# Kernel tuning notes

Hardware: AMD Instinct MI355X
Metric: run time of the kernel (lower is better)

The kernel has to match this reference:

```python
import jax, jax.numpy as jnp
import numpy as np

B, S, DIM = 2, 2048, 2048
NH, NKV = 16, 16
HD = 128            # constructor head_dim (full per-head dim, = 2 * self.head_dim)
HHD = HD // 2       # self.head_dim = per-stream dim = 64
ROPE_THETA = 10000.0
LAMBDA_INIT = 0.8 - 0.6 * float(np.exp(-0.3 * 0))  # block_id = 0 -> 0.2
EPS = 1e-5


def make_freq_cis(seq_len, dim, theta):
    # rotation matrices, shape (seq, dim//2, 2, 2): [[cos, -sin], [sin, cos]]
    inv = 1.0 / (theta ** (np.arange(0, dim, 2, dtype=np.float32) / dim))
    ang = np.arange(seq_len, dtype=np.float32)[:, None] * inv[None, :]
    cos, sin = np.cos(ang), np.sin(ang)
    fc = np.stack([np.stack([cos, -sin], -1), np.stack([sin, cos], -1)], -2)
    return jnp.asarray(fc, dtype=jnp.float32)


def setup_inputs() -> dict:
    key = jax.random.key(0)
    ks = jax.random.split(key, 9)
    std = DIM ** -0.5
    return {
        "x": jax.random.normal(ks[0], (B, S, DIM), jnp.float32),
        "freq_cis": make_freq_cis(S, HD, ROPE_THETA),
        "wq": jax.random.normal(ks[1], (NH * HD, DIM), jnp.float32) * std,
        "wk": jax.random.normal(ks[2], (NKV * HD, DIM), jnp.float32) * std,
        "wv": jax.random.normal(ks[3], (NKV * HD, DIM), jnp.float32) * std,
        "wo": jax.random.normal(ks[4], (DIM, NH * HD), jnp.float32) * std,
        "lambda_q1": jax.random.normal(ks[5], (HHD,), jnp.float32) * 0.1,
        "lambda_k1": jax.random.normal(ks[6], (HHD,), jnp.float32) * 0.1,
        "lambda_q2": jax.random.normal(ks[7], (HHD,), jnp.float32) * 0.1,
        "lambda_k2": jax.random.normal(ks[8], (HHD,), jnp.float32) * 0.1,
        "subln_w": jnp.ones((HD,), jnp.float32),
    }


def _rope(t, fc):
    # t: (b, s, h, d); fc: (s, d//2, 2, 2). Pairs (even, odd) rotated by 2x2 matrix.
    b, s, h, d = t.shape
    t2 = t.reshape(b, s, h, d // 2, 1, 2)
    out = (t2 * fc[None, :, None]).sum(-1)  # (b, s, h, d//2, 2)
    return out.reshape(b, s, h, d)


def _causal_attn(q, k, v):
    # q, k: (b, s, h, HHD); v: (b, s, h, HD). Flash-attn default scale = 1/sqrt(q head dim).
    scale = 1.0 / jnp.sqrt(jnp.asarray(q.shape[-1], q.dtype))
    scores = jnp.einsum('bqhd,bkhd->bhqk', q, k) * scale
    s = q.shape[1]
    causal = jnp.tril(jnp.ones((s, s), bool))
    scores = jnp.where(causal, scores, jnp.finfo(scores.dtype).min)
    p = jax.nn.softmax(scores, axis=-1)
    return jnp.einsum('bhqk,bkhd->bqhd', p, v)  # (b, s, h, HD)


def reference(x, freq_cis, wq, wk, wv, wo, lambda_q1, lambda_k1, lambda_q2, lambda_k2, subln_w):
    b, s, _ = x.shape
    xq = (x @ wq.T).reshape(b, s, NH, HD)
    xk = (x @ wk.T).reshape(b, s, NKV, HD)
    xv = (x @ wv.T).reshape(b, s, NKV, HD)
    xq = _rope(xq, freq_cis)
    xk = _rope(xk, freq_cis)
    if NKV != NH:  # GQA: repeat kv heads group-wise
        rep = NH // NKV
        xk = jnp.repeat(xk, rep, axis=2)
        xv = jnp.repeat(xv, rep, axis=2)
    # split each head into two differential streams of size HHD
    xq = xq.reshape(b, s, NH, 2, HHD)
    xk = xk.reshape(b, s, NH, 2, HHD)
    attn1 = _causal_attn(xq[:, :, :, 0], xk[:, :, :, 0], xv)
    attn2 = _causal_attn(xq[:, :, :, 1], xk[:, :, :, 1], xv)
    lam1 = jnp.exp(jnp.sum(lambda_q1 * lambda_k1))
    lam2 = jnp.exp(jnp.sum(lambda_q2 * lambda_k2))
    lam_full = lam1 - lam2 + LAMBDA_INIT
    attn = attn1 - lam_full * attn2              # (b, s, h, HD)
    attn = jnp.transpose(attn, (0, 2, 1, 3))     # faithful to torch .transpose(1, 2)
    ms = jnp.mean(jnp.square(attn), axis=-1, keepdims=True)
    attn = attn * jax.lax.rsqrt(ms + EPS) * subln_w  # RMSNorm(2*HHD)
    attn = attn * (1.0 - LAMBDA_INIT)
    # faithful to original: reshape (b, h, s, HD) row-major into (b, s, h*HD)
    attn = attn.reshape(b, s, NH * HD)
    return attn @ wo.T
```

## Files before the change

kernel.cpp:

```cpp
#include <hip/hip_runtime.h>

typedef unsigned short u16;
typedef unsigned int   u32;
typedef __attribute__((ext_vector_type(8))) short s16x8;
typedef __attribute__((ext_vector_type(4))) float f32x4;

constexpr int Bc = 2, Sc = 2048, DIMc = 2048, NHc = 16, HDc = 128, Tc = Bc * Sc;
constexpr float LAMBDA_INIT_C = 0.2f;

__device__ __forceinline__ u16 f2bf(float f) {
  union { float f; u32 u; } v; v.f = f;
  u32 r = v.u + 0x7fffu + ((v.u >> 16) & 1u);
  return (u16)(r >> 16);
}
__device__ __forceinline__ float bf2f(u16 b) {
  union { u32 u; float f; } v; v.u = ((u32)b) << 16;
  return v.f;
}
__device__ __forceinline__ f32x4 mfma16(s16x8 a, s16x8 b, f32x4 c) {
  return __builtin_amdgcn_mfma_f32_16x16x32_bf16(a, b, c, 0, 0, 0);
}

typedef const __attribute__((address_space(1))) u32 gq32;
typedef __attribute__((address_space(3))) u32 lq32;
__device__ __forceinline__ void cp16(const u16* g, u16* l) {
  __builtin_amdgcn_global_load_lds((gq32*)g, (lq32*)l, 16, 0, 0);
}

__global__ void cvt_all_kernel(const float* __restrict__ x,
                               const float* __restrict__ wq, const float* __restrict__ wk,
                               const float* __restrict__ wv, const float* __restrict__ wo,
                               u16* __restrict__ xb, u16* __restrict__ wb) {
  const int i = blockIdx.x * 256 + threadIdx.x;
  constexpr int NX = Tc * DIMc / 4;
  constexpr int PW = DIMc * DIMc / 4;
  float4 v; uint2* dst;
  if (i < NX) {
    v = ((const float4*)x)[i];
    dst = ((uint2*)xb) + i;
  } else {
    const int j = i - NX;
    const int which = j >> 20;
    const int jj = j & (PW - 1);
    const float* src = which == 0 ? wq : which == 1 ? wk : which == 2 ? wv : wo;
    v = ((const float4*)src)[jj];
    dst = ((uint2*)wb) + j;
  }
  union { u16 u[4]; uint2 p; } o;
  o.u[0] = f2bf(v.x); o.u[1] = f2bf(v.y); o.u[2] = f2bf(v.z); o.u[3] = f2bf(v.w);
  *dst = o.p;
}

template<int MODE>
__global__ __launch_bounds__(512, 2) void gemm8p(const u16* __restrict__ A,
                                                 const u16* __restrict__ Bw,
                                                 u16* __restrict__ Cb,
                                                 float* __restrict__ Cf,
                                                 int N) {
  constexpr int K = 2048, NT = K / 64;
  constexpr int BUF = 24576;
  __shared__ __align__(16) u16 L[2 * BUF];

  const int tid  = threadIdx.x;
  const int lane = tid & 63, w = tid >> 6;
  const int wm = w >> 2, wn = w & 3;
  const int l15 = lane & 15, quad = lane >> 4;

  const int gx   = gridDim.x;
  const int nwg  = gx * gridDim.y;
  const int flat = blockIdx.y * gx + blockIdx.x;
  const int swz  = (flat & 7) * (nwg >> 3) + (flat >> 3);
  const int nbase = (swz % gx) * 256;
  const int mbase = (swz / gx) * 128;

  const u16* Ag = A  + (size_t)mbase * K;
  const u16* Bg = Bw + (size_t)nbase * K;

  u32 soff[2], dlin[2];
#pragma unroll
  for (int l = 0; l < 2; l++) {
    const int n = l * 512 + tid;
    const int r = n >> 3;
    const u32 q = (u32)((n & 7) ^ (r & 7));
    soff[l] = (u32)r * K + q * 8;
    dlin[l] = (u32)n * 8;
  }

  auto stA = [&](int kt, int bb) {
#pragma unroll
    for (int l = 0; l < 2; l++)
      cp16(Ag + (size_t)kt * 64 + soff[l], L + bb + dlin[l]);
  };
  auto stB = [&](int kt, int h, int bb) {
#pragma unroll
    for (int l = 0; l < 2; l++)
      cp16(Bg + (size_t)h * (128 * K) + (size_t)kt * 64 + soff[l],
           L + bb + 8192 + h * 8192 + dlin[l]);
  };

  const int aB  = (wm * 64 + l15) * 64;
  const int bB  = 8192 + (wn * 64 + l15) * 64;
  const int xq0 = (quad ^ (l15 & 7)) << 3;

  f32x4 acc[4][4];
#pragma unroll
  for (int i = 0; i < 4; i++)
#pragma unroll
    for (int j = 0; j < 4; j++) acc[i][j] = (f32x4){0.f, 0.f, 0.f, 0.f};

  stB(0, 0, 0); stB(0, 1, 0); stA(0, 0); stB(1, 0, BUF); stB(1, 1, BUF);
  asm volatile("s_waitcnt vmcnt(4)" ::: "memory");
  asm volatile("s_barrier" ::: "memory");

  s16x8 aL[2][2], aH[2][2], b0[2][2], b1[2][2];

  for (int kt = 0; kt < NT; ++kt) {
    const int cb  = (kt & 1) * BUF;
    const int nb  = BUF - cb;
    const int tgA = (kt + 1 < NT) ? kt + 1 : 0;
    const int tgB = (kt + 2 < NT) ? kt + 2 : 0;

#pragma unroll
    for (int i = 0; i < 2; i++) {
      aL[i][0] = *(const s16x8*)(L + cb + aB + i * 1024 + xq0);
      aL[i][1] = *(const s16x8*)(L + cb + aB + i * 1024 + (xq0 ^ 32));
    }
#pragma unroll
    for (int j = 0; j < 2; j++) {
      b0[j][0] = *(const s16x8*)(L + cb + bB + j * 1024 + xq0);
      b0[j][1] = *(const s16x8*)(L + cb + bB + j * 1024 + (xq0 ^ 32));
    }
    stA(tgA, nb);
    asm volatile("s_barrier" ::: "memory");
    asm volatile("s_waitcnt lgkmcnt(0)" ::: "memory");
    __builtin_amdgcn_sched_barrier(0);
    __builtin_amdgcn_s_setprio(1);
#pragma unroll
    for (int i = 0; i < 2; i++)
#pragma unroll
      for (int j = 0; j < 2; j++) {
        acc[i][j] = mfma16(aL[i][0], b0[j][0], acc[i][j]);
        acc[i][j] = mfma16(aL[i][1], b0[j][1], acc[i][j]);
      }
    __builtin_amdgcn_s_setprio(0);
    asm volatile("s_barrier" ::: "memory");

#pragma unroll
    for (int j = 0; j < 2; j++) {
      b1[j][0] = *(const s16x8*)(L + cb + bB + (j + 2) * 1024 + xq0);
      b1[j][1] = *(const s16x8*)(L + cb + bB + (j + 2) * 1024 + (xq0 ^ 32));
    }
    asm volatile("s_barrier" ::: "memory");
    asm volatile("s_waitcnt lgkmcnt(0)" ::: "memory");
    __builtin_amdgcn_sched_barrier(0);
    __builtin_amdgcn_s_setprio(1);
#pragma unroll
    for (int i = 0; i < 2; i++)
#pragma unroll
      for (int j = 0; j < 2; j++) {
        acc[i][j + 2] = mfma16(aL[i][0], b1[j][0], acc[i][j + 2]);
        acc[i][j + 2] = mfma16(aL[i][1], b1[j][1], acc[i][j + 2]);
      }
    __builtin_amdgcn_s_setprio(0);
    asm volatile("s_barrier" ::: "memory");

#pragma unroll
    for (int i = 0; i < 2; i++) {
      aH[i][0] = *(const s16x8*)(L + cb + aB + (i + 2) * 1024 + xq0);
      aH[i][1] = *(const s16x8*)(L + cb + aB + (i + 2) * 1024 + (xq0 ^ 32));
    }
    stB(tgB, 0, cb);
    asm volatile("s_barrier" ::: "memory");
    asm volatile("s_waitcnt lgkmcnt(0)" ::: "memory");
    __builtin_amdgcn_sched_barrier(0);
    __builtin_amdgcn_s_setprio(1);
#pragma unroll
    for (int i = 0; i < 2; i++)
#pragma unroll
      for (int j = 0; j < 2; j++) {
        acc[i + 2][j + 2] = mfma16(aH[i][0], b1[j][0], acc[i + 2][j + 2]);
        acc[i + 2][j + 2] = mfma16(aH[i][1], b1[j][1], acc[i + 2][j + 2]);
      }
    __builtin_amdgcn_s_setprio(0);
    asm volatile("s_barrier" ::: "memory");

    stB(tgB, 1, cb);
    asm volatile("s_waitcnt vmcnt(4)" ::: "memory");
    asm volatile("s_barrier" ::: "memory");
    __builtin_amdgcn_sched_barrier(0);
    __builtin_amdgcn_s_setprio(1);
#pragma unroll
    for (int i = 0; i < 2; i++)
#pragma unroll
      for (int j = 0; j < 2; j++) {
        acc[i + 2][j] = mfma16(aH[i][0], b0[j][0], acc[i + 2][j]);
        acc[i + 2][j] = mfma16(aH[i][1], b0[j][1], acc[i + 2][j]);
      }
    __builtin_amdgcn_s_setprio(0);
    asm volatile("s_barrier" ::: "memory");
  }
  asm volatile("s_waitcnt vmcnt(0)" ::: "memory");

  if (MODE == 0) {
    const int which = nbase >> 11;
    const int ncol  = nbase & 2047;
    u16* Ob = Cb + (size_t)which * ((size_t)Tc * DIMc);
#pragma unroll
    for (int i = 0; i < 4; i++) {
      const int m0 = mbase + wm * 64 + i * 16 + quad * 4;
#pragma unroll
      for (int j = 0; j < 4; j++) {
        const int n0 = ncol + wn * 64 + j * 16 + l15;
#pragma unroll
        for (int r = 0; r < 4; r++)
          Ob[(size_t)(m0 + r) * 2048 + n0] = f2bf(acc[i][j][r]);
      }
    }
  } else {
#pragma unroll
    for (int i = 0; i < 4; i++) {
      const int m0 = mbase + wm * 64 + i * 16 + quad * 4;
#pragma unroll
      for (int j = 0; j < 4; j++) {
        const int n0 = nbase + wn * 64 + j * 16 + l15;
#pragma unroll
        for (int r = 0; r < 4; r++)
          Cf[(size_t)(m0 + r) * N + n0] = acc[i][j][r];
      }
    }
  }
}

__global__ void prep_kernel(const u16* __restrict__ qg, const u16* __restrict__ kg,
                            const u16* __restrict__ vg, const float* __restrict__ fc,
                            u16* __restrict__ qr, u16* __restrict__ kr,
                            u16* __restrict__ vt) {
  __shared__ u16 tile[32][33];
  const int bid = blockIdx.x;
  if (bid < 32768) {
    const bool isq = bid < 16384;
    const u16* xg = isq ? qg : kg;
    u16* outp = isq ? qr : kr;
    const float scale = isq ? 0.125f : 1.0f;
    const int idx = (bid & 16383) * 256 + threadIdx.x;
    const int p = idx & 63;
    const int hh = (idx >> 6) & 15;
    const int tt = idx >> 10;
    const int s = tt & (Sc - 1);
    const int bb = tt >> 11;
    const float c  = fc[(size_t)(s * 64 + p) * 4 + 0] * scale;
    const float sn = fc[(size_t)(s * 64 + p) * 4 + 2] * scale;
    const u32 xp = *(const u32*)(xg + (size_t)tt * DIMc + hh * HDc + p * 2);
    const float x0 = bf2f((u16)xp), x1 = bf2f((u16)(xp >> 16));
    const u16 y0 = f2bf(c * x0 - sn * x1);
    const u16 y1 = f2bf(sn * x0 + c * x1);
    *(u32*)(outp + ((size_t)(bb * NHc + hh) * Sc + s) * HDc + p * 2) =
        (u32)y0 | ((u32)y1 << 16);
  } else {
    const int vb = bid - 32768;
    const int bh = vb >> 8;
    const int bb = bh >> 4, hh = bh & 15;
    const int rem = vb & 255;
    const int s0 = (rem & 63) * 32, d0 = (rem >> 6) * 32;
    const int tx = threadIdx.x & 31, ty = threadIdx.x >> 5;
#pragma unroll
    for (int pp = 0; pp < 4; pp++) {
      const int s = s0 + ty + pp * 8;
      tile[ty + pp * 8][tx] = vg[(size_t)(bb * Sc + s) * DIMc + hh * HDc + d0 + tx];
    }
    __syncthreads();
#pragma unroll
    for (int pp = 0; pp < 4; pp++) {
      const int d = d0 + ty + pp * 8;
      vt[((size_t)bh * HDc + d) * Sc + s0 + tx] = tile[tx][ty + pp * 8];
    }
  }
}

__global__ __launch_bounds__(256, 2) void diff_attn_kernel(
    const u16* __restrict__ qr, const u16* __restrict__ kr, const u16* __restrict__ vt,
    const float* __restrict__ lq1, const float* __restrict__ lk1,
    const float* __restrict__ lq2, const float* __restrict__ lk2,
    const float* __restrict__ subw, u16* __restrict__ Y) {
  __shared__ u16 KB[2][8192];
  __shared__ u16 VB[2][8192];

  const int h = blockIdx.y, b = blockIdx.z, jb = blockIdx.x;
  const int bh = b * NHc + h;
  const int tid = threadIdx.x;
  const int w = tid >> 6, lane = tid & 63;
  const int l15 = lane & 15, quad = lane >> 4;

  const u16* krb = kr + (size_t)bh * Sc * HDc;
  const u16* vtb = vt + (size_t)bh * HDc * Sc;

  float lp1 = lq1[lane] * lk1[lane];
  float lp2 = lq2[lane] * lk2[lane];
#pragma unroll
  for (int m = 32; m; m >>= 1) { lp1 += __shfl_xor(lp1, m); lp2 += __shfl_xor(lp2, m); }
  const float lam = __expf(lp1) - __expf(lp2) + LAMBDA_INIT_C;

  float wsub[8];
#pragma unroll
  for (int dn = 0; dn < 8; dn++) wsub[dn] = subw[dn * 16 + l15];

  size_t offK[4], offV[4];
  int dstO[4];
#pragma unroll
  for (int oo = 0; oo < 4; oo++) {
    const int n = w * 256 + oo * 64 + lane;
    const int s = n & 31, dblk = (n >> 5) & 15, sub = n >> 9;
    const int mkey = (s & 3) + ((s >> 2) & 3) * 8 + ((s >> 4) << 2);
    offK[oo] = (size_t)(sub * 32 + mkey) * HDc + dblk * 8;
    offV[oo] = (size_t)(n & 127) * Sc + (sub * 32 + ((n >> 7) & 3) * 8);
    dstO[oo] = n * 8;
  }

  for (int ph = 0; ph < 2; ph++) {
    const int t = ph ? (31 - jb) : jb;
    const int rowbase = t * 64 + w * 16;
    const int nc = t + 1;

    const u16* qp = qr + ((size_t)bh * Sc + rowbase + l15) * HDc + quad * 8;
    s16x8 qa[2][2];
    qa[0][0] = *(const s16x8*)(qp);
    qa[0][1] = *(const s16x8*)(qp + 32);
    qa[1][0] = *(const s16x8*)(qp + 64);
    qa[1][1] = *(const s16x8*)(qp + 96);

    f32x4 o[2][8];
#pragma unroll
    for (int st = 0; st < 2; st++)
#pragma unroll
      for (int dn = 0; dn < 8; dn++) o[st][dn] = (f32x4){0.f, 0.f, 0.f, 0.f};
    float lpart[2] = { 0.f, 0.f };

    __syncthreads();
#pragma unroll
    for (int oo = 0; oo < 4; oo++) cp16(krb + offK[oo], KB[0] + dstO[oo]);
#pragma unroll
    for (int oo = 0; oo < 4; oo++) cp16(vtb + offV[oo], VB[0] + dstO[oo]);

    for (int c = 0; c < nc; c++) {
      __syncthreads();
      if (c + 1 < nc) {
        const int kb1 = (c + 1) * 64;
        u16* Kn = KB[(c + 1) & 1];
        u16* Vn = VB[(c + 1) & 1];
#pragma unroll
        for (int oo = 0; oo < 4; oo++) cp16(krb + (size_t)kb1 * HDc + offK[oo], Kn + dstO[oo]);
#pragma unroll
        for (int oo = 0; oo < 4; oo++) cp16(vtb + offV[oo] + kb1, Vn + dstO[oo]);
      }
      const u16* Kb = KB[c & 1];
      const u16* Vb = VB[c & 1];
      const int kb = c * 64;
      const bool diag = (c == nc - 1);

#pragma unroll
      for (int sub = 0; sub < 2; sub++) {
        if (diag && sub == 1 && w < 2) continue;

        f32x4 sc[2][2];
#pragma unroll
        for (int st = 0; st < 2; st++)
#pragma unroll
          for (int kt = 0; kt < 2; kt++) sc[st][kt] = (f32x4){0.f, 0.f, 0.f, 0.f};
#pragma unroll
        for (int st = 0; st < 2; st++)
#pragma unroll
          for (int kh = 0; kh < 2; kh++) {
            const int base = sub * 512 + (st * 8 + kh * 4 + quad) * 32;
#pragma unroll
            for (int kt = 0; kt < 2; kt++) {
              const s16x8 kf = *(const s16x8*)(Kb + (size_t)(base + kt * 16 + l15) * 8);
              sc[st][kt] = mfma16(kf, qa[st][kh], sc[st][kt]);
            }
          }

        s16x8 pa[2];
#pragma unroll
        for (int st = 0; st < 2; st++) {
          float p[8];
#pragma unroll
          for (int kt = 0; kt < 2; kt++)
#pragma unroll
            for (int r = 0; r < 4; r++) p[kt * 4 + r] = __expf(sc[st][kt][r]);
          if (diag) {
            const int qrow = rowbase + l15;
            const int kb0 = kb + sub * 32 + quad * 8;
#pragma unroll
            for (int j8 = 0; j8 < 8; j8++)
              if (kb0 + j8 > qrow) p[j8] = 0.f;
          }
          float sm = 0.f;
#pragma unroll
          for (int j8 = 0; j8 < 8; j8++) sm += p[j8];
          lpart[st] += sm;
          union { u16 us[8]; s16x8 vv; } pk;
#pragma unroll
          for (int j8 = 0; j8 < 8; j8++) pk.us[j8] = f2bf(p[j8]);
          pa[st] = pk.vv;
        }

#pragma unroll
        for (int dn = 0; dn < 8; dn++) {
          const s16x8 vf =
              *(const s16x8*)(Vb + (size_t)(sub * 512 + quad * 128 + dn * 16 + l15) * 8);
          o[0][dn] = mfma16(pa[0], vf, o[0][dn]);
          o[1][dn] = mfma16(pa[1], vf, o[1][dn]);
        }
      }
    }

    float lL0 = lpart[0], lL1 = lpart[1];
    lL0 += __shfl_xor(lL0, 16); lL0 += __shfl_xor(lL0, 32);
    lL1 += __shfl_xor(lL1, 16); lL1 += __shfl_xor(lL1, 32);
    const float inv1 = 1.f / lL0;
    const float inv2 = lam / lL1;
    float i1C[4], i2C[4];
#pragma unroll
    for (int r = 0; r < 4; r++) {
      i1C[r] = __shfl(inv1, quad * 4 + r, 16);
      i2C[r] = __shfl(inv2, quad * 4 + r, 16);
    }
    float yv[8][4], ss[4] = { 0.f, 0.f, 0.f, 0.f };
#pragma unroll
    for (int dn = 0; dn < 8; dn++)
#pragma unroll
      for (int r = 0; r < 4; r++) {
        const float y = o[0][dn][r] * i1C[r] - o[1][dn][r] * i2C[r];
        yv[dn][r] = y;
        ss[r] += y * y;
      }
#pragma unroll
    for (int r = 0; r < 4; r++) {
#pragma unroll
      for (int mm = 1; mm < 16; mm <<= 1) ss[r] += __shfl_xor(ss[r], mm);
    }
    float scl[4];
#pragma unroll
    for (int r = 0; r < 4; r++) scl[r] = rsqrtf(ss[r] * (1.f / 128.f) + 1e-5f) * 0.8f;

    u16* yrow = Y + ((size_t)(b * Sc + h * 128 + t * 4 + w)) * 2048;
#pragma unroll
    for (int dn = 0; dn < 8; dn++)
#pragma unroll
      for (int r = 0; r < 4; r++)
        yrow[(quad * 4 + r) * 128 + dn * 16 + l15] = f2bf(yv[dn][r] * scl[r] * wsub[dn]);
  }
}

extern "C" void kernel_launch(void* const* d_in, const int* in_sizes, int n_in,
                              void* d_out, int out_size, void* d_ws, size_t ws_size,
                              hipStream_t stream) {
  const float* x    = (const float*)d_in[0];
  const float* fc   = (const float*)d_in[1];
  const float* wq   = (const float*)d_in[2];
  const float* wk   = (const float*)d_in[3];
  const float* wv   = (const float*)d_in[4];
  const float* wo   = (const float*)d_in[5];
  const float* lq1  = (const float*)d_in[6];
  const float* lk1  = (const float*)d_in[7];
  const float* lq2  = (const float*)d_in[8];
  const float* lk2  = (const float*)d_in[9];
  const float* subw = (const float*)d_in[10];
  float* out = (float*)d_out;

  char* ws = (char*)d_ws;
  constexpr size_t SZ_X  = (size_t)Tc * DIMc * 2;
  constexpr size_t SZ_W  = (size_t)DIMc * DIMc * 2;
  constexpr size_t SZ_T  = (size_t)Tc * DIMc * 2;
  u16* xb  = (u16*)(ws);
  u16* wqb = (u16*)(ws + SZ_X);
  u16* wob = (u16*)(ws + SZ_X + 3 * SZ_W);
  u16* qg  = (u16*)(ws + SZ_X + 4 * SZ_W);
  u16* kg  = (u16*)(ws + SZ_X + 4 * SZ_W + SZ_T);
  u16* vg  = (u16*)(ws + SZ_X + 4 * SZ_W + 2 * SZ_T);
  u16* qr  = (u16*)(ws + SZ_X + 4 * SZ_W + 3 * SZ_T);
  u16* kr  = (u16*)(ws + SZ_X + 4 * SZ_W + 4 * SZ_T);
  u16* vt  = (u16*)(ws + SZ_X + 4 * SZ_W + 5 * SZ_T);
  u16* Y   = (u16*)(ws + SZ_X + 4 * SZ_W + 6 * SZ_T);

  cvt_all_kernel<<<(Tc * DIMc / 4 + 4 * DIMc * DIMc / 4) / 256, 256, 0, stream>>>(
      x, wq, wk, wv, wo, xb, wqb);

  gemm8p<0><<<dim3(DIMc * 3 / 256, Tc / 128), 512, 0, stream>>>(
      xb, wqb, qg, nullptr, 3 * DIMc);

  prep_kernel<<<16384 + 16384 + 8192, 256, 0, stream>>>(qg, kg, vg, fc, qr, kr, vt);

  diff_attn_kernel<<<dim3(16, NHc, Bc), 256, 0, stream>>>(
      qr, kr, vt, lq1, lk1, lq2, lk2, subw, Y);

  gemm8p<1><<<dim3(DIMc / 256, Tc / 128), 512, 0, stream>>>(
      Y, wob, nullptr, out, DIMc);
}
```

Measured before the change: 412.7 us.

## Enlarge GEMM block tile to 256x256 with 8x4 per-wave accumulators

The bf16 GEMM grows its workgroup tile from 128x256 to 256x256. Each wave now accumulates a 128x64 sub-tile, so every B fragment read from LDS feeds twice as many MFMAs and global traffic per FLOP falls. The A and B prefetch is restructured to load whole k-tiles two steps ahead into double buffers (64 KB each), and the block-index swizzle now runs M-major. The costs are twice the LDS per block, more accumulator registers (which may drop occupancy below the declared two blocks per CU), and half as many workgroups, which can leave CUs idle on the smaller output-projection GEMM.

```diff
diff --git a/kernel.cpp b/kernel.cpp
--- a/kernel.cpp
+++ b/kernel.cpp
@@ -55,10 +55,9 @@
 __global__ __launch_bounds__(512, 2) void gemm8p(const u16* __restrict__ A,
                                                  const u16* __restrict__ Bw,
                                                  u16* __restrict__ Cb,
-                                                 float* __restrict__ Cf,
-                                                 int N) {
+                                                 float* __restrict__ Cf) {
   constexpr int K = 2048, NT = K / 64;
-  constexpr int BUF = 24576;
+  constexpr int BUF = 32768;
   __shared__ __align__(16) u16 L[2 * BUF];
 
   const int tid  = threadIdx.x;
@@ -66,19 +65,19 @@
   const int wm = w >> 2, wn = w & 3;
   const int l15 = lane & 15, quad = lane >> 4;
 
-  const int gx   = gridDim.x;
-  const int nwg  = gx * gridDim.y;
-  const int flat = blockIdx.y * gx + blockIdx.x;
+  const int mt   = gridDim.y;
+  const int nwg  = gridDim.x * mt;
+  const int flat = blockIdx.x * mt + blockIdx.y;
   const int swz  = (flat & 7) * (nwg >> 3) + (flat >> 3);
-  const int nbase = (swz % gx) * 256;
-  const int mbase = (swz / gx) * 128;
+  const int nbase = (swz / mt) * 256;
+  const int mbase = (swz % mt) * 256;
 
   const u16* Ag = A  + (size_t)mbase * K;
   const u16* Bg = Bw + (size_t)nbase * K;
 
-  u32 soff[2], dlin[2];
-#pragma unroll
-  for (int l = 0; l < 2; l++) {
+  u32 soff[4], dlin[4];
+#pragma unroll
+  for (int l = 0; l < 4; l++) {
     const int n = l * 512 + tid;
     const int r = n >> 3;
     const u32 q = (u32)((n & 7) ^ (r & 7));
@@ -88,59 +87,55 @@
 
   auto stA = [&](int kt, int bb) {
 #pragma unroll
-    for (int l = 0; l < 2; l++)
+    for (int l = 0; l < 4; l++)
       cp16(Ag + (size_t)kt * 64 + soff[l], L + bb + dlin[l]);
   };
-  auto stB = [&](int kt, int h, int bb) {
-#pragma unroll
-    for (int l = 0; l < 2; l++)
-      cp16(Bg + (size_t)h * (128 * K) + (size_t)kt * 64 + soff[l],
-           L + bb + 8192 + h * 8192 + dlin[l]);
+  auto stB = [&](int kt, int bb) {
+#pragma unroll
+    for (int l = 0; l < 4; l++)
+      cp16(Bg + (size_t)kt * 64 + soff[l], L + bb + 16384 + dlin[l]);
   };
 
-  const int aB  = (wm * 64 + l15) * 64;
-  const int bB  = 8192 + (wn * 64 + l15) * 64;
+  const int aB  = (wm * 128 + l15) * 64;
+  const int bB  = 16384 + (wn * 64 + l15) * 64;
   const int xq0 = (quad ^ (l15 & 7)) << 3;
 
-  f32x4 acc[4][4];
-#pragma unroll
-  for (int i = 0; i < 4; i++)
+  f32x4 acc[8][4];
+#pragma unroll
+  for (int i = 0; i < 8; i++)
 #pragma unroll
     for (int j = 0; j < 4; j++) acc[i][j] = (f32x4){0.f, 0.f, 0.f, 0.f};
 
-  stB(0, 0, 0); stB(0, 1, 0); stA(0, 0); stB(1, 0, BUF); stB(1, 1, BUF);
-  asm volatile("s_waitcnt vmcnt(4)" ::: "memory");
+  stB(0, 0); stA(0, 0); stB(1, BUF); stA(1, BUF);
+  asm volatile("s_waitcnt vmcnt(8)" ::: "memory");
   asm volatile("s_barrier" ::: "memory");
 
-  s16x8 aL[2][2], aH[2][2], b0[2][2], b1[2][2];
+  s16x8 a[4][2], b0[2][2], b1[2][2];
 
   for (int kt = 0; kt < NT; ++kt) {
-    const int cb  = (kt & 1) * BUF;
-    const int nb  = BUF - cb;
-    const int tgA = (kt + 1 < NT) ? kt + 1 : 0;
-    const int tgB = (kt + 2 < NT) ? kt + 2 : 0;
-
-#pragma unroll
-    for (int i = 0; i < 2; i++) {
-      aL[i][0] = *(const s16x8*)(L + cb + aB + i * 1024 + xq0);
-      aL[i][1] = *(const s16x8*)(L + cb + aB + i * 1024 + (xq0 ^ 32));
+    const int cb = (kt & 1) * BUF;
+    const int tg = (kt + 2 < NT) ? kt + 2 : 0;
+
+#pragma unroll
+    for (int i = 0; i < 4; i++) {
+      a[i][0] = *(const s16x8*)(L + cb + aB + i * 1024 + xq0);
+      a[i][1] = *(const s16x8*)(L + cb + aB + i * 1024 + (xq0 ^ 32));
     }
 #pragma unroll
     for (int j = 0; j < 2; j++) {
       b0[j][0] = *(const s16x8*)(L + cb + bB + j * 1024 + xq0);
       b0[j][1] = *(const s16x8*)(L + cb + bB + j * 1024 + (xq0 ^ 32));
     }
-    stA(tgA, nb);
     asm volatile("s_barrier" ::: "memory");
     asm volatile("s_waitcnt lgkmcnt(0)" ::: "memory");
     __builtin_amdgcn_sched_barrier(0);
     __builtin_amdgcn_s_setprio(1);
 #pragma unroll
-    for (int i = 0; i < 2; i++)
+    for (int i = 0; i < 4; i++)
 #pragma unroll
       for (int j = 0; j < 2; j++) {
-        acc[i][j] = mfma16(aL[i][0], b0[j][0], acc[i][j]);
-        acc[i][j] = mfma16(aL[i][1], b0[j][1], acc[i][j]);
+        acc[i][j] = mfma16(a[i][0], b0[j][0], acc[i][j]);
+        acc[i][j] = mfma16(a[i][1], b0[j][1], acc[i][j]);
       }
     __builtin_amdgcn_s_setprio(0);
     asm volatile("s_barrier" ::: "memory");
@@ -155,46 +150,46 @@
     __builtin_amdgcn_sched_barrier(0);
     __builtin_amdgcn_s_setprio(1);
 #pragma unroll
-    for (int i = 0; i < 2; i++)
+    for (int i = 0; i < 4; i++)
 #pragma unroll
       for (int j = 0; j < 2; j++) {
-        acc[i][j + 2] = mfma16(aL[i][0], b1[j][0], acc[i][j + 2]);
-        acc[i][j + 2] = mfma16(aL[i][1], b1[j][1], acc[i][j + 2]);
+        acc[i][j + 2] = mfma16(a[i][0], b1[j][0], acc[i][j + 2]);
+        acc[i][j + 2] = mfma16(a[i][1], b1[j][1], acc[i][j + 2]);
       }
     __builtin_amdgcn_s_setprio(0);
     asm volatile("s_barrier" ::: "memory");
 
 #pragma unroll
-    for (int i = 0; i < 2; i++) {
-      aH[i][0] = *(const s16x8*)(L + cb + aB + (i + 2) * 1024 + xq0);
-      aH[i][1] = *(const s16x8*)(L + cb + aB + (i + 2) * 1024 + (xq0 ^ 32));
-    }
-    stB(tgB, 0, cb);
+    for (int i = 0; i < 4; i++) {
+      a[i][0] = *(const s16x8*)(L + cb + aB + 4096 + i * 1024 + xq0);
+      a[i][1] = *(const s16x8*)(L + cb + aB + 4096 + i * 1024 + (xq0 ^ 32));
+    }
+    stB(tg, cb);
     asm volatile("s_barrier" ::: "memory");
     asm volatile("s_waitcnt lgkmcnt(0)" ::: "memory");
     __builtin_amdgcn_sched_barrier(0);
     __builtin_amdgcn_s_setprio(1);
 #pragma unroll
-    for (int i = 0; i < 2; i++)
+    for (int i = 0; i < 4; i++)
 #pragma unroll
       for (int j = 0; j < 2; j++) {
-        acc[i + 2][j + 2] = mfma16(aH[i][0], b1[j][0], acc[i + 2][j + 2]);
-        acc[i + 2][j + 2] = mfma16(aH[i][1], b1[j][1], acc[i + 2][j + 2]);
+        acc[i + 4][j + 2] = mfma16(a[i][0], b1[j][0], acc[i + 4][j + 2]);
+        acc[i + 4][j + 2] = mfma16(a[i][1], b1[j][1], acc[i + 4][j + 2]);
       }
     __builtin_amdgcn_s_setprio(0);
     asm volatile("s_barrier" ::: "memory");
 
-    stB(tgB, 1, cb);
-    asm volatile("s_waitcnt vmcnt(4)" ::: "memory");
+    stA(tg, cb);
+    asm volatile("s_waitcnt vmcnt(8)" ::: "memory");
     asm volatile("s_barrier" ::: "memory");
     __builtin_amdgcn_sched_barrier(0);
     __builtin_amdgcn_s_setprio(1);
 #pragma unroll
-    for (int i = 0; i < 2; i++)
+    for (int i = 0; i < 4; i++)
 #pragma unroll
       for (int j = 0; j < 2; j++) {
-        acc[i + 2][j] = mfma16(aH[i][0], b0[j][0], acc[i + 2][j]);
-        acc[i + 2][j] = mfma16(aH[i][1], b0[j][1], acc[i + 2][j]);
+        acc[i + 4][j] = mfma16(a[i][0], b0[j][0], acc[i + 4][j]);
+        acc[i + 4][j] = mfma16(a[i][1], b0[j][1], acc[i + 4][j]);
       }
     __builtin_amdgcn_s_setprio(0);
     asm volatile("s_barrier" ::: "memory");
@@ -206,8 +201,8 @@
     const int ncol  = nbase & 2047;
     u16* Ob = Cb + (size_t)which * ((size_t)Tc * DIMc);
 #pragma unroll
-    for (int i = 0; i < 4; i++) {
-      const int m0 = mbase + wm * 64 + i * 16 + quad * 4;
+    for (int i = 0; i < 8; i++) {
+      const int m0 = mbase + wm * 128 + i * 16 + quad * 4;
 #pragma unroll
       for (int j = 0; j < 4; j++) {
         const int n0 = ncol + wn * 64 + j * 16 + l15;
@@ -218,14 +213,14 @@
     }
   } else {
 #pragma unroll
-    for (int i = 0; i < 4; i++) {
-      const int m0 = mbase + wm * 64 + i * 16 + quad * 4;
+    for (int i = 0; i < 8; i++) {
+      const int m0 = mbase + wm * 128 + i * 16 + quad * 4;
 #pragma unroll
       for (int j = 0; j < 4; j++) {
         const int n0 = nbase + wn * 64 + j * 16 + l15;
 #pragma unroll
         for (int r = 0; r < 4; r++)
-          Cf[(size_t)(m0 + r) * N + n0] = acc[i][j][r];
+          Cf[(size_t)(m0 + r) * 2048 + n0] = acc[i][j][r];
       }
     }
   }
@@ -485,14 +480,14 @@
   cvt_all_kernel<<<(Tc * DIMc / 4 + 4 * DIMc * DIMc / 4) / 256, 256, 0, stream>>>(
       x, wq, wk, wv, wo, xb, wqb);
 
-  gemm8p<0><<<dim3(DIMc * 3 / 256, Tc / 128), 512, 0, stream>>>(
-      xb, wqb, qg, nullptr, 3 * DIMc);
+  gemm8p<0><<<dim3(DIMc * 3 / 256, Tc / 256), 512, 0, stream>>>(
+      xb, wqb, qg, nullptr);
 
   prep_kernel<<<16384 + 16384 + 8192, 256, 0, stream>>>(qg, kg, vg, fc, qr, kr, vt);
 
   diff_attn_kernel<<<dim3(16, NHc, Bc), 256, 0, stream>>>(
       qr, kr, vt, lq1, lk1, lq2, lk2, subw, Y);
 
-  gemm8p<1><<<dim3(DIMc / 256, Tc / 128), 512, 0, stream>>>(
-      Y, wob, nullptr, out, DIMc);
-}
+  gemm8p<1><<<dim3(DIMc / 256, Tc / 256), 512, 0, stream>>>(
+      Y, wob, nullptr, out);
+}
```

Measured after the change: 439.3 us. 1.06x slower.
